# Kernel tuning notes

Hardware: AMD Instinct MI355X
Metric: run time of the kernel (lower is better)

The kernel has to match this reference:

```python
import jax, jax.numpy as jnp
import numpy as np

DINO_SHIFT = 0.7
COEF = 1.0
EPS = 1e-12


def setup_inputs() -> dict:
    key = jax.random.key(0)
    k1, k2 = jax.random.split(key)
    N, H, W, C, K = 2, 48, 48, 384, 16
    dino_feature_map = jax.random.normal(k1, (N, H, W, C), dtype=jnp.float32)
    # relevance map in log space (log-probabilities over classes)
    log_p_class = jax.nn.log_softmax(jax.random.normal(k2, (N, H, W, K), dtype=jnp.float32), axis=-1)
    dino_pos_weight = jnp.ones((1,), dtype=jnp.float32)
    dino_neg_weight = jnp.ones((1,), dtype=jnp.float32)
    return {
        "dino_feature_map": dino_feature_map,
        "log_p_class": log_p_class,
        "dino_pos_weight": dino_pos_weight,
        "dino_neg_weight": dino_neg_weight,
    }


def _normalize(x):
    # F.normalize(x, dim=-1): x / max(||x||, eps)
    n = jnp.sqrt(jnp.sum(x * x, axis=-1, keepdims=True))
    return x / jnp.maximum(n, EPS)


def _js_correlation(a, b):
    # a, b: [N, L, C] log-probs. Pairwise JS divergence matrix [N, L, L].
    # Same math as the torch broadcast version, but the sum over C is
    # factored into einsums so the [N,L,L,C] tensor is never materialized:
    #   kl_am[s,l] = sum_c e^{a[s,c]} a[s,c] - sum_c e^{a[s,c]} m[l,c]
    m = jnp.logaddexp(a, b) - jnp.log(2.0)           # [N, L, C]
    ea = jnp.exp(a)
    kl_am = jnp.sum(ea * a, axis=-1)[:, :, None] - jnp.einsum('nsc,nlc->nsl', ea, m)
    eb = jnp.exp(b)
    kl_bm = jnp.sum(eb * b, axis=-1)[:, :, None] - jnp.einsum('nsc,nlc->nsl', eb, m)
    return (kl_am + kl_bm) / 2.0


def _fda_loss(feats, log_p, pw, nw):
    N = feats.shape[0]
    f = feats.reshape(N, -1, feats.shape[-1])          # [N, HW, C]
    p = log_p.reshape(N, -1, log_p.shape[-1])          # [N, HW, K]
    fn = _normalize(f)
    f_corr = jnp.einsum('nsc,nlc->nsl', fn, fn) - DINO_SHIFT
    f_corr = jax.lax.stop_gradient(f_corr)             # torch.no_grad block
    f_pos = jnp.maximum(f_corr, 0.0)
    f_neg = jnp.minimum(f_corr, 0.0)
    p_corr = _js_correlation(p, p)                     # [N, HW, HW]
    n_pos = jnp.count_nonzero(f_pos).astype(f_pos.dtype)
    n_neg = jnp.count_nonzero(f_neg).astype(f_neg.dtype)
    pos_loss = jnp.sum(f_pos * p_corr) / n_pos
    neg_loss = jnp.sum(f_neg * p_corr) / n_neg
    loss = pos_loss * pw[0] + neg_loss * nw[0]
    return loss * COEF                                 # reduction='none' on a scalar


def reference(dino_feature_map, log_p_class, dino_pos_weight, dino_neg_weight):
    return _fda_loss(dino_feature_map, log_p_class, dino_pos_weight, dino_neg_weight)
```

## Files before the change

kernel.cpp:

```cpp
#include <hip/hip_runtime.h>
#include <math.h>
#include <stdint.h>

#define NN 2
#define LL 2304
#define CC 384
#define KK 16
#define DINO_SHIFT 0.7f

#define NT 24
#define TB 96
#define TT ((NT * (NT + 1)) / 2)
#define NBLK2 (NN * TT)

typedef __attribute__((ext_vector_type(8))) short short8;
typedef __attribute__((ext_vector_type(4))) float f32x4;

#define AS_G __attribute__((address_space(1)))
#define AS_L __attribute__((address_space(3)))

__device__ __forceinline__ unsigned short f2bf(float x) {
    union { float f; uint32_t u; } v; v.f = x;
    uint32_t r = v.u + 0x7fffu + ((v.u >> 16) & 1u);
    return (unsigned short)(r >> 16);
}

__device__ __forceinline__ void gll16(const void* g, void* l) {
    __builtin_amdgcn_global_load_lds((const AS_G unsigned int*)g,
                                     (AS_L unsigned int*)l, 16, 0, 0);
}

__global__ void prep_kernel(const float* __restrict__ f, const float* __restrict__ p,
                            unsigned short* __restrict__ fnorm,
                            unsigned short* __restrict__ Ppad,
                            unsigned short* __restrict__ ppad,
                            float* __restrict__ selfdot) {
    const int r = blockIdx.x * 4 + (threadIdx.x >> 6);
    const int lane = threadIdx.x & 63;
    const float* frow = f + (size_t)r * CC;
    float v[6], ss = 0.f;
#pragma unroll
    for (int k = 0; k < 6; ++k) { v[k] = frow[lane + 64 * k]; ss = fmaf(v[k], v[k], ss); }
#pragma unroll
    for (int off = 32; off; off >>= 1) ss += __shfl_xor(ss, off);
    const float rn = 1.0f / fmaxf(sqrtf(ss), 1e-12f);
    unsigned short* fnr = fnorm + (size_t)r * CC;
#pragma unroll
    for (int k = 0; k < 6; ++k) fnr[lane + 64 * k] = f2bf(v[k] * rn);

    if (lane < 32) {
        float pv = 0.f, e = 0.f;
        if (lane < KK) { pv = p[(size_t)r * KK + lane]; e = expf(pv); }
        Ppad[(size_t)r * 32 + lane] = (lane < KK) ? f2bf(e)  : (unsigned short)0;
        ppad[(size_t)r * 32 + lane] = (lane < KK) ? f2bf(pv) : (unsigned short)0;
        float sd = e * pv;
#pragma unroll
        for (int off = 8; off; off >>= 1) sd += __shfl_xor(sd, off, 16);
        if (lane == 0) selfdot[r] = sd;
    }
}

__global__ __launch_bounds__(256, 2) void pair_kernel(
    const unsigned short* __restrict__ fnorm,
    const unsigned short* __restrict__ Ppad, const unsigned short* __restrict__ ppad,
    const float* __restrict__ selfdot, float* __restrict__ partials)
{
    __shared__ char lds[49152] __attribute__((aligned(16)));
    __shared__ float red[4][4];

    const int b = blockIdx.x;
    const int n = b / TT;
    int t = b % TT;
    int i = 0;
    while (t >= NT - i) { t -= NT - i; ++i; }
    const int j = i + t;
    const int s0 = i * TB, l0 = j * TB;
    const bool diag = (i == j);
    const float wgt = diag ? 1.f : 2.f;

    const int tid = threadIdx.x, lane = tid & 63, w = tid >> 6;
    const int wrow = w >> 1, wcol = w & 1;

    const unsigned short* fn = fnorm + (size_t)n * LL * CC;
    const int srow8 = lane >> 3, sch = lane & 7;

    f32x4 acc[3][3] = {};

    auto stageF = [&](int buf, int c0) {
        char* base = lds + buf * 24576;
#pragma unroll
        for (int q = 0; q < 3; ++q) {
            const int r0 = w * 24 + q * 8;
            const int row = r0 + srow8;
            const char* src = (const char*)(fn + (size_t)(s0 + row) * CC) + c0 * 2
                              + ((sch ^ (row & 7)) << 4);
            gll16(src, base + r0 * 128);
        }
        if (!diag) {
#pragma unroll
            for (int q = 0; q < 3; ++q) {
                const int r0 = w * 24 + q * 8;
                const int row = r0 + srow8;
                const char* src = (const char*)(fn + (size_t)(l0 + row) * CC) + c0 * 2
                                  + ((sch ^ (row & 7)) << 4);
                gll16(src, base + 12288 + r0 * 128);
            }
        }
    };

    stageF(0, 0);
    asm volatile("s_waitcnt vmcnt(0)" ::: "memory");
    __syncthreads();

#pragma unroll 2
    for (int tt = 0; tt < 6; ++tt) {
        if (tt < 5) stageF((tt + 1) & 1, (tt + 1) * 64);
        const char* abase = lds + (tt & 1) * 24576;
        const char* bbase = diag ? abase : abase + 12288;
#pragma unroll
        for (int ks = 0; ks < 2; ++ks) {
            short8 a[3], bb[3];
#pragma unroll
            for (int im = 0; im < 3; ++im) {
                const int row = wrow * 48 + im * 16 + (lane & 15);
                a[im] = *(const short8*)(abase + row * 128
                         + (((ks * 4 + (lane >> 4)) ^ (row & 7)) << 4));
            }
#pragma unroll
            for (int jn = 0; jn < 3; ++jn) {
                const int row = wcol * 48 + jn * 16 + (lane & 15);
                bb[jn] = *(const short8*)(bbase + row * 128
                         + (((ks * 4 + (lane >> 4)) ^ (row & 7)) << 4));
            }
#pragma unroll
            for (int im = 0; im < 3; ++im)
#pragma unroll
                for (int jn = 0; jn < 3; ++jn)
                    acc[im][jn] = __builtin_amdgcn_mfma_f32_16x16x32_bf16(
                        a[im], bb[jn], acc[im][jn], 0, 0, 0);
        }
        asm volatile("s_waitcnt vmcnt(0)" ::: "memory");
        __syncthreads();
    }

    {
        const char* Pb = (const char*)Ppad + (size_t)(n * LL + s0) * 64;
        const char* pb = (const char*)ppad + (size_t)(n * LL + l0) * 64;
        const int erow = lane >> 2, ech = lane & 3;
#pragma unroll
        for (int q3 = 0; q3 < 3; ++q3) {
            const int q = w * 3 + q3;
            const int qq = (q < 6) ? q : q - 6;
            const int row = qq * 16 + erow;
            const char* sb = (q < 6) ? Pb : pb;
            gll16(sb + row * 64 + ((ech ^ (row & 3)) << 4),
                  lds + ((q < 6) ? 0 : 12288) + qq * 1024);
        }
    }
    asm volatile("s_waitcnt vmcnt(0)" ::: "memory");
    __syncthreads();

    short8 a2[3], b2[3];
#pragma unroll
    for (int im = 0; im < 3; ++im) {
        const int row = wrow * 48 + im * 16 + (lane & 15);
        a2[im] = *(const short8*)(lds + row * 64 + (((lane >> 4) ^ (row & 3)) << 4));
    }
#pragma unroll
    for (int jn = 0; jn < 3; ++jn) {
        const int row = wcol * 48 + jn * 16 + (lane & 15);
        b2[jn] = *(const short8*)(lds + 12288 + row * 64 + (((lane >> 4) ^ (row & 3)) << 4));
    }

    float pos = 0.f, neg = 0.f, npc = 0.f, nnc = 0.f;
#pragma unroll
    for (int im = 0; im < 3; ++im) {
        const f32x4 sd4 = *(const f32x4*)(selfdot + (size_t)n * LL + s0
                            + wrow * 48 + im * 16 + ((lane >> 4) << 2));
#pragma unroll
        for (int jn = 0; jn < 3; ++jn) {
            f32x4 z = {0.f, 0.f, 0.f, 0.f};
            f32x4 pdv = __builtin_amdgcn_mfma_f32_16x16x32_bf16(a2[im], b2[jn], z, 0, 0, 0);
#pragma unroll
            for (int r = 0; r < 4; ++r) {
                const float fc = acc[im][jn][r] - DINO_SHIFT;
                const float pc = sd4[r] - pdv[r];
                const float v = fc * pc;
                if (fc > 0.f)      { pos += v; npc += 1.f; }
                else if (fc < 0.f) { neg += v; nnc += 1.f; }
            }
        }
    }
    pos *= wgt; neg *= wgt; npc *= wgt; nnc *= wgt;

#pragma unroll
    for (int off = 32; off; off >>= 1) {
        pos += __shfl_xor(pos, off); neg += __shfl_xor(neg, off);
        npc += __shfl_xor(npc, off); nnc += __shfl_xor(nnc, off);
    }
    if (lane == 0) { red[w][0] = pos; red[w][1] = neg; red[w][2] = npc; red[w][3] = nnc; }
    __syncthreads();
    if (tid == 0) {
        partials[b * 4 + 0] = red[0][0] + red[1][0] + red[2][0] + red[3][0];
        partials[b * 4 + 1] = red[0][1] + red[1][1] + red[2][1] + red[3][1];
        partials[b * 4 + 2] = red[0][2] + red[1][2] + red[2][2] + red[3][2];
        partials[b * 4 + 3] = red[0][3] + red[1][3] + red[2][3] + red[3][3];
    }
}

__global__ void final_kernel(const float* __restrict__ partials,
                             const float* __restrict__ pw,
                             const float* __restrict__ nw,
                             float* __restrict__ out) {
    __shared__ float red[4][4];
    const int tid = threadIdx.x;
    float pos = 0.f, neg = 0.f, np = 0.f, nn = 0.f;
    for (int i = tid; i < NBLK2; i += 256) {
        pos += partials[i * 4 + 0];
        neg += partials[i * 4 + 1];
        np  += partials[i * 4 + 2];
        nn  += partials[i * 4 + 3];
    }
#pragma unroll
    for (int off = 32; off; off >>= 1) {
        pos += __shfl_xor(pos, off); neg += __shfl_xor(neg, off);
        np  += __shfl_xor(np, off);  nn  += __shfl_xor(nn, off);
    }
    const int w = tid >> 6, lane = tid & 63;
    if (lane == 0) { red[w][0] = pos; red[w][1] = neg; red[w][2] = np; red[w][3] = nn; }
    __syncthreads();
    if (tid == 0) {
        pos = red[0][0] + red[1][0] + red[2][0] + red[3][0];
        neg = red[0][1] + red[1][1] + red[2][1] + red[3][1];
        np  = red[0][2] + red[1][2] + red[2][2] + red[3][2];
        nn  = red[0][3] + red[1][3] + red[2][3] + red[3][3];
        out[0] = (pos / np) * pw[0] + (neg / nn) * nw[0];
    }
}

extern "C" void kernel_launch(void* const* d_in, const int* in_sizes, int n_in,
                              void* d_out, int out_size, void* d_ws, size_t ws_size,
                              hipStream_t stream) {
    const float* f  = (const float*)d_in[0];
    const float* p  = (const float*)d_in[1];
    const float* pw = (const float*)d_in[2];
    const float* nw = (const float*)d_in[3];
    float* out = (float*)d_out;

    unsigned short* fnorm = (unsigned short*)d_ws;
    unsigned short* Ppad  = fnorm + (size_t)NN * LL * CC;
    unsigned short* ppad  = Ppad + (size_t)NN * LL * 32;
    float* selfdot = (float*)(ppad + (size_t)NN * LL * 32);
    float* partials = selfdot + (size_t)NN * LL;

    prep_kernel<<<(NN * LL) / 4, 256, 0, stream>>>(f, p, fnorm, Ppad, ppad, selfdot);
    pair_kernel<<<NBLK2, 256, 0, stream>>>(fnorm, Ppad, ppad, selfdot, partials);
    final_kernel<<<1, 256, 0, stream>>>(partials, pw, nw, out);
}
```

Before: 25.05 us.

## Fuse final reduction into pair kernel via last-block atomic, overlap P staging

Result: slower. 33.14 us (+32.3%).

```diff
diff --git a/kernel.cpp b/kernel.cpp
--- a/kernel.cpp
+++ b/kernel.cpp
@@ -15,6 +15,7 @@
 
 typedef __attribute__((ext_vector_type(8))) short short8;
 typedef __attribute__((ext_vector_type(4))) float f32x4;
+typedef __attribute__((ext_vector_type(2))) float f32x2;
 
 #define AS_G __attribute__((address_space(1)))
 #define AS_L __attribute__((address_space(3)))
@@ -24,6 +25,9 @@
     uint32_t r = v.u + 0x7fffu + ((v.u >> 16) & 1u);
     return (unsigned short)(r >> 16);
 }
+__device__ __forceinline__ unsigned int pk2(float a, float b) {
+    return (unsigned int)f2bf(a) | ((unsigned int)f2bf(b) << 16);
+}
 
 __device__ __forceinline__ void gll16(const void* g, void* l) {
     __builtin_amdgcn_global_load_lds((const AS_G unsigned int*)g,
@@ -34,19 +38,26 @@
                             unsigned short* __restrict__ fnorm,
                             unsigned short* __restrict__ Ppad,
                             unsigned short* __restrict__ ppad,
-                            float* __restrict__ selfdot) {
+                            float* __restrict__ selfdot,
+                            unsigned int* __restrict__ counter) {
+    if (blockIdx.x == 0 && threadIdx.x == 0) counter[0] = 0u;
     const int r = blockIdx.x * 4 + (threadIdx.x >> 6);
     const int lane = threadIdx.x & 63;
-    const float* frow = f + (size_t)r * CC;
-    float v[6], ss = 0.f;
-#pragma unroll
-    for (int k = 0; k < 6; ++k) { v[k] = frow[lane + 64 * k]; ss = fmaf(v[k], v[k], ss); }
+    const f32x2* frow2 = (const f32x2*)(f + (size_t)r * CC);
+    f32x2 v[3];
+    float ss = 0.f;
+#pragma unroll
+    for (int k = 0; k < 3; ++k) {
+        v[k] = frow2[lane + 64 * k];
+        ss = fmaf(v[k][0], v[k][0], fmaf(v[k][1], v[k][1], ss));
+    }
 #pragma unroll
     for (int off = 32; off; off >>= 1) ss += __shfl_xor(ss, off);
     const float rn = 1.0f / fmaxf(sqrtf(ss), 1e-12f);
-    unsigned short* fnr = fnorm + (size_t)r * CC;
-#pragma unroll
-    for (int k = 0; k < 6; ++k) fnr[lane + 64 * k] = f2bf(v[k] * rn);
+    unsigned int* fnr32 = (unsigned int*)(fnorm + (size_t)r * CC);
+#pragma unroll
+    for (int k = 0; k < 3; ++k)
+        fnr32[lane + 64 * k] = pk2(v[k][0] * rn, v[k][1] * rn);
 
     if (lane < 32) {
         float pv = 0.f, e = 0.f;
@@ -63,12 +74,16 @@
 __global__ __launch_bounds__(256, 2) void pair_kernel(
     const unsigned short* __restrict__ fnorm,
     const unsigned short* __restrict__ Ppad, const unsigned short* __restrict__ ppad,
-    const float* __restrict__ selfdot, float* __restrict__ partials)
+    const float* __restrict__ selfdot, float* __restrict__ partials,
+    unsigned int* __restrict__ counter,
+    const float* __restrict__ pw, const float* __restrict__ nw,
+    float* __restrict__ out)
 {
     __shared__ char lds[49152] __attribute__((aligned(16)));
     __shared__ float red[4][4];
-
-    const int b = blockIdx.x;
+    __shared__ unsigned int isLast;
+
+    const int b = (blockIdx.x & 7) * (NBLK2 / 8) + (blockIdx.x >> 3);
     const int n = b / TT;
     int t = b % TT;
     int i = 0;
@@ -107,43 +122,7 @@
             }
         }
     };
-
-    stageF(0, 0);
-    asm volatile("s_waitcnt vmcnt(0)" ::: "memory");
-    __syncthreads();
-
-#pragma unroll 2
-    for (int tt = 0; tt < 6; ++tt) {
-        if (tt < 5) stageF((tt + 1) & 1, (tt + 1) * 64);
-        const char* abase = lds + (tt & 1) * 24576;
-        const char* bbase = diag ? abase : abase + 12288;
-#pragma unroll
-        for (int ks = 0; ks < 2; ++ks) {
-            short8 a[3], bb[3];
-#pragma unroll
-            for (int im = 0; im < 3; ++im) {
-                const int row = wrow * 48 + im * 16 + (lane & 15);
-                a[im] = *(const short8*)(abase + row * 128
-                         + (((ks * 4 + (lane >> 4)) ^ (row & 7)) << 4));
-            }
-#pragma unroll
-            for (int jn = 0; jn < 3; ++jn) {
-                const int row = wcol * 48 + jn * 16 + (lane & 15);
-                bb[jn] = *(const short8*)(bbase + row * 128
-                         + (((ks * 4 + (lane >> 4)) ^ (row & 7)) << 4));
-            }
-#pragma unroll
-            for (int im = 0; im < 3; ++im)
-#pragma unroll
-                for (int jn = 0; jn < 3; ++jn)
-                    acc[im][jn] = __builtin_amdgcn_mfma_f32_16x16x32_bf16(
-                        a[im], bb[jn], acc[im][jn], 0, 0, 0);
-        }
-        asm volatile("s_waitcnt vmcnt(0)" ::: "memory");
-        __syncthreads();
-    }
-
-    {
+    auto stagePP = [&]() {
         const char* Pb = (const char*)Ppad + (size_t)(n * LL + s0) * 64;
         const char* pb = (const char*)ppad + (size_t)(n * LL + l0) * 64;
         const int erow = lane >> 2, ech = lane & 3;
@@ -154,11 +133,45 @@
             const int row = qq * 16 + erow;
             const char* sb = (q < 6) ? Pb : pb;
             gll16(sb + row * 64 + ((ech ^ (row & 3)) << 4),
-                  lds + ((q < 6) ? 0 : 12288) + qq * 1024);
-        }
-    }
+                  lds + ((q < 6) ? 0 : 6144) + qq * 1024);
+        }
+    };
+
+    stageF(0, 0);
     asm volatile("s_waitcnt vmcnt(0)" ::: "memory");
     __syncthreads();
+
+#pragma unroll
+    for (int tt = 0; tt < 6; ++tt) {
+        if (tt < 5) stageF((tt + 1) & 1, (tt + 1) * 64);
+        else        stagePP();
+        const char* abase = lds + (tt & 1) * 24576;
+        const char* bbase = diag ? abase : abase + 12288;
+#pragma unroll
+        for (int ks = 0; ks < 2; ++ks) {
+            short8 a[3], bb[3];
+#pragma unroll
+            for (int im = 0; im < 3; ++im) {
+                const int row = wrow * 48 + im * 16 + (lane & 15);
+                a[im] = *(const short8*)(abase + row * 128
+                         + (((ks * 4 + (lane >> 4)) ^ (row & 7)) << 4));
+            }
+#pragma unroll
+            for (int jn = 0; jn < 3; ++jn) {
+                const int row = wcol * 48 + jn * 16 + (lane & 15);
+                bb[jn] = *(const short8*)(bbase + row * 128
+                         + (((ks * 4 + (lane >> 4)) ^ (row & 7)) << 4));
+            }
+#pragma unroll
+            for (int im = 0; im < 3; ++im)
+#pragma unroll
+                for (int jn = 0; jn < 3; ++jn)
+                    acc[im][jn] = __builtin_amdgcn_mfma_f32_16x16x32_bf16(
+                        a[im], bb[jn], acc[im][jn], 0, 0, 0);
+        }
+        asm volatile("s_waitcnt vmcnt(0)" ::: "memory");
+        __syncthreads();
+    }
 
     short8 a2[3], b2[3];
 #pragma unroll
@@ -169,7 +182,7 @@
 #pragma unroll
     for (int jn = 0; jn < 3; ++jn) {
         const int row = wcol * 48 + jn * 16 + (lane & 15);
-        b2[jn] = *(const short8*)(lds + 12288 + row * 64 + (((lane >> 4) ^ (row & 3)) << 4));
+        b2[jn] = *(const short8*)(lds + 6144 + row * 64 + (((lane >> 4) ^ (row & 3)) << 4));
     }
 
     float pos = 0.f, neg = 0.f, npc = 0.f, nnc = 0.f;
@@ -205,36 +218,25 @@
         partials[b * 4 + 1] = red[0][1] + red[1][1] + red[2][1] + red[3][1];
         partials[b * 4 + 2] = red[0][2] + red[1][2] + red[2][2] + red[3][2];
         partials[b * 4 + 3] = red[0][3] + red[1][3] + red[2][3] + red[3][3];
-    }
-}
-
-__global__ void final_kernel(const float* __restrict__ partials,
-                             const float* __restrict__ pw,
-                             const float* __restrict__ nw,
-                             float* __restrict__ out) {
-    __shared__ float red[4][4];
-    const int tid = threadIdx.x;
-    float pos = 0.f, neg = 0.f, np = 0.f, nn = 0.f;
-    for (int i = tid; i < NBLK2; i += 256) {
-        pos += partials[i * 4 + 0];
-        neg += partials[i * 4 + 1];
-        np  += partials[i * 4 + 2];
-        nn  += partials[i * 4 + 3];
-    }
-#pragma unroll
-    for (int off = 32; off; off >>= 1) {
-        pos += __shfl_xor(pos, off); neg += __shfl_xor(neg, off);
-        np  += __shfl_xor(np, off);  nn  += __shfl_xor(nn, off);
-    }
-    const int w = tid >> 6, lane = tid & 63;
-    if (lane == 0) { red[w][0] = pos; red[w][1] = neg; red[w][2] = np; red[w][3] = nn; }
+        __threadfence();
+        unsigned int r = atomicAdd(counter, 1u);
+        isLast = (r == NBLK2 - 1) ? 1u : 0u;
+    }
     __syncthreads();
-    if (tid == 0) {
-        pos = red[0][0] + red[1][0] + red[2][0] + red[3][0];
-        neg = red[0][1] + red[1][1] + red[2][1] + red[3][1];
-        np  = red[0][2] + red[1][2] + red[2][2] + red[3][2];
-        nn  = red[0][3] + red[1][3] + red[2][3] + red[3][3];
-        out[0] = (pos / np) * pw[0] + (neg / nn) * nw[0];
+
+    if (isLast && tid < 64) {
+        __threadfence();
+        float ps = 0.f, ng = 0.f, np = 0.f, nn = 0.f;
+        for (int q = tid; q < NBLK2; q += 64) {
+            const f32x4 v = *(const f32x4*)(partials + q * 4);
+            ps += v[0]; ng += v[1]; np += v[2]; nn += v[3];
+        }
+#pragma unroll
+        for (int off = 32; off; off >>= 1) {
+            ps += __shfl_xor(ps, off); ng += __shfl_xor(ng, off);
+            np += __shfl_xor(np, off); nn += __shfl_xor(nn, off);
+        }
+        if (tid == 0) out[0] = (ps / np) * pw[0] + (ng / nn) * nw[0];
     }
 }
 
@@ -250,10 +252,11 @@
     unsigned short* fnorm = (unsigned short*)d_ws;
     unsigned short* Ppad  = fnorm + (size_t)NN * LL * CC;
     unsigned short* ppad  = Ppad + (size_t)NN * LL * 32;
-    float* selfdot = (float*)(ppad + (size_t)NN * LL * 32);
+    float* selfdot  = (float*)(ppad + (size_t)NN * LL * 32);
     float* partials = selfdot + (size_t)NN * LL;
-
-    prep_kernel<<<(NN * LL) / 4, 256, 0, stream>>>(f, p, fnorm, Ppad, ppad, selfdot);
-    pair_kernel<<<NBLK2, 256, 0, stream>>>(fnorm, Ppad, ppad, selfdot, partials);
-    final_kernel<<<1, 256, 0, stream>>>(partials, pw, nw, out);
-}
+    unsigned int* counter = (unsigned int*)(partials + (size_t)NBLK2 * 4);
+
+    prep_kernel<<<(NN * LL) / 4, 256, 0, stream>>>(f, p, fnorm, Ppad, ppad, selfdot, counter);
+    pair_kernel<<<NBLK2, 256, 0, stream>>>(fnorm, Ppad, ppad, selfdot, partials,
+                                           counter, pw, nw, out);
+}
```

## Triple-buffer the K loop with vmcnt-counted prefetch and overlap P tile staging

Applied to the files above, without the earlier changes.

Measured after the change: 29.48 us. 1.18x slower.

```diff
diff --git a/kernel.cpp b/kernel.cpp
--- a/kernel.cpp
+++ b/kernel.cpp
@@ -15,6 +15,7 @@
 
 typedef __attribute__((ext_vector_type(8))) short short8;
 typedef __attribute__((ext_vector_type(4))) float f32x4;
+typedef __attribute__((ext_vector_type(2))) float f32x2;
 
 #define AS_G __attribute__((address_space(1)))
 #define AS_L __attribute__((address_space(3)))
@@ -23,6 +24,9 @@
     union { float f; uint32_t u; } v; v.f = x;
     uint32_t r = v.u + 0x7fffu + ((v.u >> 16) & 1u);
     return (unsigned short)(r >> 16);
+}
+__device__ __forceinline__ unsigned int pk2(float a, float b) {
+    return (unsigned int)f2bf(a) | ((unsigned int)f2bf(b) << 16);
 }
 
 __device__ __forceinline__ void gll16(const void* g, void* l) {
@@ -37,16 +41,21 @@
                             float* __restrict__ selfdot) {
     const int r = blockIdx.x * 4 + (threadIdx.x >> 6);
     const int lane = threadIdx.x & 63;
-    const float* frow = f + (size_t)r * CC;
-    float v[6], ss = 0.f;
-#pragma unroll
-    for (int k = 0; k < 6; ++k) { v[k] = frow[lane + 64 * k]; ss = fmaf(v[k], v[k], ss); }
+    const f32x2* frow2 = (const f32x2*)(f + (size_t)r * CC);
+    f32x2 v[3];
+    float ss = 0.f;
+#pragma unroll
+    for (int k = 0; k < 3; ++k) {
+        v[k] = frow2[lane + 64 * k];
+        ss = fmaf(v[k][0], v[k][0], fmaf(v[k][1], v[k][1], ss));
+    }
 #pragma unroll
     for (int off = 32; off; off >>= 1) ss += __shfl_xor(ss, off);
     const float rn = 1.0f / fmaxf(sqrtf(ss), 1e-12f);
-    unsigned short* fnr = fnorm + (size_t)r * CC;
-#pragma unroll
-    for (int k = 0; k < 6; ++k) fnr[lane + 64 * k] = f2bf(v[k] * rn);
+    unsigned int* fnr32 = (unsigned int*)(fnorm + (size_t)r * CC);
+#pragma unroll
+    for (int k = 0; k < 3; ++k)
+        fnr32[lane + 64 * k] = pk2(v[k][0] * rn, v[k][1] * rn);
 
     if (lane < 32) {
         float pv = 0.f, e = 0.f;
@@ -65,7 +74,7 @@
     const unsigned short* __restrict__ Ppad, const unsigned short* __restrict__ ppad,
     const float* __restrict__ selfdot, float* __restrict__ partials)
 {
-    __shared__ char lds[49152] __attribute__((aligned(16)));
+    __shared__ char lds[73728] __attribute__((aligned(16)));
     __shared__ float red[4][4];
 
     const int b = blockIdx.x;
@@ -75,8 +84,7 @@
     while (t >= NT - i) { t -= NT - i; ++i; }
     const int j = i + t;
     const int s0 = i * TB, l0 = j * TB;
-    const bool diag = (i == j);
-    const float wgt = diag ? 1.f : 2.f;
+    const float wgt = (i == j) ? 1.f : 2.f;
 
     const int tid = threadIdx.x, lane = tid & 63, w = tid >> 6;
     const int wrow = w >> 1, wcol = w & 1;
@@ -86,64 +94,20 @@
 
     f32x4 acc[3][3] = {};
 
-    auto stageF = [&](int buf, int c0) {
+    auto stageF = [&](int buf, int kt) {
         char* base = lds + buf * 24576;
 #pragma unroll
         for (int q = 0; q < 3; ++q) {
             const int r0 = w * 24 + q * 8;
             const int row = r0 + srow8;
-            const char* src = (const char*)(fn + (size_t)(s0 + row) * CC) + c0 * 2
-                              + ((sch ^ (row & 7)) << 4);
-            gll16(src, base + r0 * 128);
-        }
-        if (!diag) {
-#pragma unroll
-            for (int q = 0; q < 3; ++q) {
-                const int r0 = w * 24 + q * 8;
-                const int row = r0 + srow8;
-                const char* src = (const char*)(fn + (size_t)(l0 + row) * CC) + c0 * 2
-                                  + ((sch ^ (row & 7)) << 4);
-                gll16(src, base + 12288 + r0 * 128);
-            }
+            const int swz = (sch ^ (row & 7)) << 4;
+            gll16((const char*)(fn + (size_t)(s0 + row) * CC) + kt * 128 + swz,
+                  base + r0 * 128);
+            gll16((const char*)(fn + (size_t)(l0 + row) * CC) + kt * 128 + swz,
+                  base + 12288 + r0 * 128);
         }
     };
-
-    stageF(0, 0);
-    asm volatile("s_waitcnt vmcnt(0)" ::: "memory");
-    __syncthreads();
-
-#pragma unroll 2
-    for (int tt = 0; tt < 6; ++tt) {
-        if (tt < 5) stageF((tt + 1) & 1, (tt + 1) * 64);
-        const char* abase = lds + (tt & 1) * 24576;
-        const char* bbase = diag ? abase : abase + 12288;
-#pragma unroll
-        for (int ks = 0; ks < 2; ++ks) {
-            short8 a[3], bb[3];
-#pragma unroll
-            for (int im = 0; im < 3; ++im) {
-                const int row = wrow * 48 + im * 16 + (lane & 15);
-                a[im] = *(const short8*)(abase + row * 128
-                         + (((ks * 4 + (lane >> 4)) ^ (row & 7)) << 4));
-            }
-#pragma unroll
-            for (int jn = 0; jn < 3; ++jn) {
-                const int row = wcol * 48 + jn * 16 + (lane & 15);
-                bb[jn] = *(const short8*)(bbase + row * 128
-                         + (((ks * 4 + (lane >> 4)) ^ (row & 7)) << 4));
-            }
-#pragma unroll
-            for (int im = 0; im < 3; ++im)
-#pragma unroll
-                for (int jn = 0; jn < 3; ++jn)
-                    acc[im][jn] = __builtin_amdgcn_mfma_f32_16x16x32_bf16(
-                        a[im], bb[jn], acc[im][jn], 0, 0, 0);
-        }
-        asm volatile("s_waitcnt vmcnt(0)" ::: "memory");
-        __syncthreads();
-    }
-
-    {
+    auto stagePP = [&]() {
         const char* Pb = (const char*)Ppad + (size_t)(n * LL + s0) * 64;
         const char* pb = (const char*)ppad + (size_t)(n * LL + l0) * 64;
         const int erow = lane >> 2, ech = lane & 3;
@@ -154,11 +118,54 @@
             const int row = qq * 16 + erow;
             const char* sb = (q < 6) ? Pb : pb;
             gll16(sb + row * 64 + ((ech ^ (row & 3)) << 4),
-                  lds + ((q < 6) ? 0 : 12288) + qq * 1024);
-        }
-    }
+                  lds + ((q < 6) ? 0 : 6144) + qq * 1024);
+        }
+    };
+    auto compute = [&](int buf) {
+        const char* abase = lds + buf * 24576;
+        const char* bbase = abase + 12288;
+#pragma unroll
+        for (int ks = 0; ks < 2; ++ks) {
+            short8 a[3], bb[3];
+#pragma unroll
+            for (int im = 0; im < 3; ++im) {
+                const int row = wrow * 48 + im * 16 + (lane & 15);
+                a[im] = *(const short8*)(abase + row * 128
+                         + (((ks * 4 + (lane >> 4)) ^ (row & 7)) << 4));
+            }
+#pragma unroll
+            for (int jn = 0; jn < 3; ++jn) {
+                const int row = wcol * 48 + jn * 16 + (lane & 15);
+                bb[jn] = *(const short8*)(bbase + row * 128
+                         + (((ks * 4 + (lane >> 4)) ^ (row & 7)) << 4));
+            }
+#pragma unroll
+            for (int im = 0; im < 3; ++im)
+#pragma unroll
+                for (int jn = 0; jn < 3; ++jn)
+                    acc[im][jn] = __builtin_amdgcn_mfma_f32_16x16x32_bf16(
+                        a[im], bb[jn], acc[im][jn], 0, 0, 0);
+        }
+    };
+
+    stageF(0, 0);
+    stageF(1, 1);
+#define K_ITER(TT_I, VMC) \
+    { if (TT_I < 4) stageF((TT_I + 2) % 3, TT_I + 2); \
+      else if (TT_I == 4) stagePP(); \
+      asm volatile("s_waitcnt vmcnt(" #VMC ")" ::: "memory"); \
+      asm volatile("s_barrier" ::: "memory"); \
+      compute(TT_I % 3); \
+      asm volatile("s_barrier" ::: "memory"); }
+    K_ITER(0, 12)
+    K_ITER(1, 12)
+    K_ITER(2, 12)
+    K_ITER(3, 12)
+    K_ITER(4, 9)
+    K_ITER(5, 3)
+#undef K_ITER
     asm volatile("s_waitcnt vmcnt(0)" ::: "memory");
-    __syncthreads();
+    asm volatile("s_barrier" ::: "memory");
 
     short8 a2[3], b2[3];
 #pragma unroll
@@ -169,7 +176,7 @@
 #pragma unroll
     for (int jn = 0; jn < 3; ++jn) {
         const int row = wcol * 48 + jn * 16 + (lane & 15);
-        b2[jn] = *(const short8*)(lds + 12288 + row * 64 + (((lane >> 4) ^ (row & 3)) << 4));
+        b2[jn] = *(const short8*)(lds + 6144 + row * 64 + (((lane >> 4) ^ (row & 3)) << 4));
     }
 
     float pos = 0.f, neg = 0.f, npc = 0.f, nnc = 0.f;
@@ -216,10 +223,8 @@
     const int tid = threadIdx.x;
     float pos = 0.f, neg = 0.f, np = 0.f, nn = 0.f;
     for (int i = tid; i < NBLK2; i += 256) {
-        pos += partials[i * 4 + 0];
-        neg += partials[i * 4 + 1];
-        np  += partials[i * 4 + 2];
-        nn  += partials[i * 4 + 3];
+        const f32x4 v = *(const f32x4*)(partials + i * 4);
+        pos += v[0]; neg += v[1]; np += v[2]; nn += v[3];
     }
 #pragma unroll
     for (int off = 32; off; off >>= 1) {
@@ -250,7 +255,7 @@
     unsigned short* fnorm = (unsigned short*)d_ws;
     unsigned short* Ppad  = fnorm + (size_t)NN * LL * CC;
     unsigned short* ppad  = Ppad + (size_t)NN * LL * 32;
-    float* selfdot = (float*)(ppad + (size_t)NN * LL * 32);
+    float* selfdot  = (float*)(ppad + (size_t)NN * LL * 32);
     float* partials = selfdot + (size_t)NN * LL;
 
     prep_kernel<<<(NN * LL) / 4, 256, 0, stream>>>(f, p, fnorm, Ppad, ppad, selfdot);
```
